# Kernel tuning notes

Hardware: AMD Instinct MI355X
Metric: run time of the kernel (lower is better)

Reference implementation:

```python
import jax, jax.numpy as jnp
import numpy as np
import math

IN_FEATURES = 1024
OUT_FEATURES = 1024
GRID_SIZE = 5
SPLINE_ORDER = 3
BATCH = 4096
K = GRID_SIZE + 2 * SPLINE_ORDER  # 11 basis functions per feature


def make_grid():
    h = (1.0 - (-1.0)) / GRID_SIZE
    xx = np.arange(-SPLINE_ORDER, GRID_SIZE + SPLINE_ORDER + 1, dtype=np.float32) * h + (-1.0)
    return jnp.asarray(np.broadcast_to(xx, (IN_FEATURES, xx.shape[0])).copy())  # (in, K+1)


def setup_inputs() -> dict:
    key = jax.random.key(0)
    k1, k2, k3, k4 = jax.random.split(key, 4)
    x = jax.random.normal(k1, (BATCH, IN_FEATURES), dtype=jnp.float32)
    base_weight = jax.random.normal(k2, (OUT_FEATURES, IN_FEATURES), dtype=jnp.float32) * 0.02
    spline_weight = jax.random.normal(k3, (OUT_FEATURES, IN_FEATURES, K), dtype=jnp.float32) * 0.02
    spline_scaler = jax.random.normal(k4, (OUT_FEATURES, IN_FEATURES), dtype=jnp.float32) * 0.1
    return {"x": x, "base_weight": base_weight, "spline_weight": spline_weight,
            "spline_scaler": spline_scaler, "grid": make_grid()}


def trig_basis(x, grid):
    # x: (B, in) ; grid: (in, K+1) -> basis: (B, in, K)
    a = grid[:, :-1]                      # (in, K)
    b = grid[:, 1:]                       # (in, K)
    interval = jnp.maximum(b - a, 1e-8)
    xe = x[:, :, None]                    # (B, in, 1)
    inside = ((xe >= a) & (xe < b)).astype(x.dtype)
    trig = jnp.sin(jnp.pi * (xe - a) / interval)
    return inside * trig


def reference(x, base_weight, spline_weight, spline_scaler, grid):
    # base branch: SiLU(x) @ base_weight^T
    enm = jax.nn.silu(x) @ base_weight.T                     # (B, out)
    # spline branch: fused basis expansion + GEMM
    basis = trig_basis(x, grid)                              # (B, in, K)
    sw = spline_weight * spline_scaler[:, :, None]           # (out, in, K)
    snm = jnp.einsum('bik,oik->bo', basis, sw)               # (B, out)
    return enm + snm
```

## Files before the change

kernel.cpp:

```cpp
#include <hip/hip_runtime.h>
#include <hip/hip_bf16.h>

#define BATCH  4096
#define INF    1024
#define OUTF   1024
#define KSPL   11
#define KSPB   11264
#define SW_SCALE 1016.0f

using bf16    = __hip_bfloat16;
using short8  = __attribute__((ext_vector_type(8))) short;
using ushort8 = __attribute__((ext_vector_type(8))) unsigned short;
using f32x4   = __attribute__((ext_vector_type(4))) float;
using i32x4   = __attribute__((ext_vector_type(4))) int;
typedef unsigned long long u64;

__device__ __forceinline__ unsigned short f2bf(float f){
  union { float f; unsigned u; } a; a.f = f;
  return (unsigned short)((a.u + 0x7FFFu + ((a.u >> 16) & 1u)) >> 16);
}

__device__ __forceinline__ void llds16(const void* g, const void* l){
  __builtin_amdgcn_global_load_lds(
      (const __attribute__((address_space(1))) unsigned int*)g,
      (__attribute__((address_space(3))) unsigned int*)l, 16, 0, 0);
}

__device__ __forceinline__ void bar(){
  asm volatile("" ::: "memory");
  __builtin_amdgcn_s_barrier();
  asm volatile("" ::: "memory");
}

__device__ __forceinline__ f32x4 mfma16(short8 a, short8 b, f32x4 c){
  return __builtin_amdgcn_mfma_f32_16x16x32_bf16(a, b, c, 0, 0, 0);
}
__device__ __forceinline__ i32x4 mfma_i8(i32x4 a, i32x4 b, i32x4 c){
  return __builtin_amdgcn_mfma_i32_16x16x64_i8(a, b, c, 0, 0, 0);
}

__device__ __forceinline__ int swz(int L){ return L ^ (((L>>7)&7)<<4); }

__global__ __launch_bounds__(256) void prep(const float* __restrict__ x,
                                            const float* __restrict__ bw,
                                            const float* __restrict__ sw,
                                            const float* __restrict__ sc,
                                            bf16* __restrict__ A_sil,
                                            char* __restrict__ A_spl,
                                            bf16* __restrict__ W_b,
                                            char* __restrict__ W_s){
  const int t = threadIdx.x;
  if (blockIdx.x < 2048){
    const int gid = blockIdx.x * 256 + t;
    const int b  = gid >> 7;
    const int i0 = (gid & 127) * 8;
    const float* xr = x + (size_t)b * INF + i0;
    f32x4 p0 = *(const f32x4*)xr;
    f32x4 p1 = *(const f32x4*)(xr + 4);
    float v[8];
    #pragma unroll
    for (int j = 0; j < 4; ++j){ v[j] = p0[j]; v[4+j] = p1[j]; }
    ushort8 sl;
    int c[8], q[8];
    #pragma unroll
    for (int j = 0; j < 8; ++j){
      float xx = v[j];
      sl[j] = f2bf(xx / (1.0f + __expf(-xx)));
      float tt = (xx + 1.0f) * 2.5f;
      float fl = floorf(tt);
      c[j] = (int)fl + 3;
      q[j] = (int)rintf(__sinf(3.14159265358979f * (tt - fl)) * 127.0f);
    }
    *(ushort8*)(A_sil + (size_t)b*INF + i0) = sl;
    char* ar = A_spl + (size_t)b * KSPB + i0;
    #pragma unroll
    for (int k = 0; k < KSPL; ++k){
      u64 up = 0;
      #pragma unroll
      for (int j = 0; j < 8; ++j){
        unsigned char byte = (c[j] == k) ? (unsigned char)q[j] : (unsigned char)0;
        up |= ((u64)byte) << (8*j);
      }
      *(u64*)(ar + k*INF) = up;
    }
  } else {
    const int gid = (blockIdx.x - 2048) * 256 + t;
    const int o  = gid >> 7;
    const int i0 = (gid & 127) * 8;
    float buf[88];
    const float* sp = sw + ((size_t)o*INF + i0) * KSPL;
    #pragma unroll
    for (int qd = 0; qd < 22; ++qd)
      ((f32x4*)buf)[qd] = ((const f32x4*)sp)[qd];
    f32x4 c0 = *(const f32x4*)(sc + (size_t)o*INF + i0);
    f32x4 c1 = *(const f32x4*)(sc + (size_t)o*INF + i0 + 4);
    float scv[8];
    #pragma unroll
    for (int j = 0; j < 4; ++j){ scv[j] = c0[j]; scv[4+j] = c1[j]; }
    {
      const float* br = bw + (size_t)o*INF + i0;
      f32x4 v0 = *(const f32x4*)br;
      f32x4 v1 = *(const f32x4*)(br + 4);
      ushort8 u;
      #pragma unroll
      for (int j = 0; j < 4; ++j){ u[j] = f2bf(v0[j]); u[4+j] = f2bf(v1[j]); }
      *(ushort8*)(W_b + (size_t)o*INF + i0) = u;
    }
    char* wr = W_s + (size_t)o * KSPB + i0;
    #pragma unroll
    for (int k = 0; k < KSPL; ++k){
      u64 up = 0;
      #pragma unroll
      for (int j = 0; j < 8; ++j){
        float vv = buf[j*KSPL + k] * scv[j] * SW_SCALE;
        vv = fminf(fmaxf(vv, -127.0f), 127.0f);
        int qq = (int)rintf(vv);
        up |= ((u64)(unsigned char)(signed char)qq) << (8*j);
      }
      *(u64*)(wr + k*INF) = up;
    }
  }
}

template<int NS>
__global__ __launch_bounds__(512, 2) void gemm_i8k(const char* __restrict__ A,
                                                   const char* __restrict__ W,
                                                   int* __restrict__ Cp){
  constexpr int KSPLIT_B = KSPB / NS;
  constexpr int NG       = KSPLIT_B / 64;
  __shared__ __align__(16) char smem[131072];

  const int bid = blockIdx.x;
  const int xcd = bid & 7, local = bid >> 3;
  const int split = xcd >> 1;
  const int mt    = (xcd & 1) * 8 + (local >> 2);
  const int nt    = local & 3;
  const int bm = mt*256, bn = nt*256;

  const int t    = threadIdx.x;
  const int lane = t & 63, w = t >> 6;
  const int wr = w >> 2, wc = w & 3;
  const int r15 = lane & 15, hi = lane >> 4;

  int offA[8], offB[4];
  #pragma unroll
  for (int m = 0; m < 8; ++m){
    int L = (wr*128 + m*16 + r15)*64 + hi*16;
    offA[m] = swz(L);
  }
  #pragma unroll
  for (int n = 0; n < 4; ++n){
    int L = (wc*64 + n*16 + r15)*64 + hi*16;
    offB[n] = 16384 + swz(L);
  }

  const char* gA[2]; const char* gB[2];
  int ldsA[2], ldsB[2];
  #pragma unroll
  for (int j = 0; j < 2; ++j){
    int P = (t + j*512)*16;
    int L = swz(P);
    int row = L >> 6, inner = L & 63;
    gA[j] = A + (size_t)(bm + row)*KSPB + split*KSPLIT_B + inner;
    gB[j] = W + (size_t)(bn + row)*KSPB + split*KSPLIT_B + inner;
    ldsA[j] = j*8192 + w*1024;
    ldsB[j] = 16384 + j*8192 + w*1024;
  }

  #define STAGE(buf, tile) do{ \
    llds16(gA[0] + (tile)*64, smem + (buf)*32768 + ldsA[0]); \
    llds16(gA[1] + (tile)*64, smem + (buf)*32768 + ldsA[1]); \
    llds16(gB[0] + (tile)*64, smem + (buf)*32768 + ldsB[0]); \
    llds16(gB[1] + (tile)*64, smem + (buf)*32768 + ldsB[1]); }while(0)

  i32x4 acc[8][4] = {};
  i32x4 afA[4], afB[4], bfA[4], bfB[4];

  STAGE(0,0);
  STAGE(1,1);
  asm volatile("s_waitcnt vmcnt(4)" ::: "memory");
  bar();
  #pragma unroll
  for (int n = 0; n < 4; ++n) bfA[n] = *(const i32x4*)(smem + offB[n]);
  #pragma unroll
  for (int m = 0; m < 4; ++m) afA[m] = *(const i32x4*)(smem + offA[m]);

  #define BODY(tt, curA, curB, nxtA, nxtB) do{                                \
    const char* bp_ = smem + ((tt)&3)*32768;                                  \
    const char* bq_ = smem + (((tt)+1)&3)*32768;                              \
    if ((tt) + 2 < NG){                                                       \
      STAGE(((tt)+2)&3, (tt)+2);                                              \
      asm volatile("s_waitcnt vmcnt(4)" ::: "memory");                        \
    } else {                                                                  \
      asm volatile("s_waitcnt vmcnt(0)" ::: "memory");                        \
    }                                                                         \
    bar();                                                                    \
    i32x4 ag_[4];                                                             \
    __builtin_amdgcn_s_setprio(1);                                            \
    _Pragma("unroll")                                                         \
    for (int m = 0; m < 4; ++m){                                              \
      ag_[m] = *(const i32x4*)(bp_ + offA[4+m]);                              \
      _Pragma("unroll")                                                       \
      for (int n = 0; n < 4; ++n)                                             \
        acc[m][n] = mfma_i8(curA[m], curB[n], acc[m][n]);                     \
    }                                                                         \
    _Pragma("unroll")                                                         \
    for (int m = 0; m < 4; ++m){                                              \
      if ((tt) + 1 < NG){                                                     \
        nxtA[m] = *(const i32x4*)(bq_ + offA[m]);                             \
        nxtB[m] = *(const i32x4*)(bq_ + offB[m]);                             \
      }                                                                       \
      _Pragma("unroll")                                                       \
      for (int n = 0; n < 4; ++n)                                             \
        acc[4+m][n] = mfma_i8(ag_[m], curB[n], acc[4+m][n]);                  \
    }                                                                         \
    __builtin_amdgcn_s_setprio(0);                                            \
  }while(0)

  #pragma unroll 1
  for (int s = 0; s < NG/2; ++s){
    BODY(2*s,   afA, bfA, afB, bfB);
    BODY(2*s+1, afB, bfB, afA, bfA);
  }
  #undef BODY
  #undef STAGE

  int* outp = Cp + (size_t)split * (BATCH*OUTF);
  #pragma unroll
  for (int m = 0; m < 8; ++m){
    const int r0 = bm + wr*128 + m*16 + hi*4;
    #pragma unroll
    for (int n = 0; n < 4; ++n){
      const int cc = bn + wc*64 + n*16 + r15;
      #pragma unroll
      for (int j = 0; j < 4; ++j)
        outp[(size_t)(r0 + j) * OUTF + cc] = acc[m][n][j];
    }
  }
}

__global__ __launch_bounds__(512, 2) void gemm_e(const bf16* __restrict__ A,
                                                 const bf16* __restrict__ W,
                                                 const int* __restrict__ Cp,
                                                 float* __restrict__ out){
  constexpr int NG = 32;
  __shared__ __align__(16) char smem[65536];

  const int bid = blockIdx.x;
  const int fin = (bid & 7) * 32 + (bid >> 3);
  const int mt = fin >> 3, nt = fin & 7;
  const int bm = mt*128, bn = nt*128;

  const int t    = threadIdx.x;
  const int lane = t & 63, w = t >> 6;
  const int wr = w >> 2, wc = w & 3;
  const int r15 = lane & 15, hi = lane >> 4;

  int offA[4], offB[2];
  #pragma unroll
  for (int m = 0; m < 4; ++m){
    int L = (wr*64 + m*16 + r15)*64 + hi*16;
    offA[m] = swz(L);
  }
  #pragma unroll
  for (int n = 0; n < 2; ++n){
    int L = (wc*32 + n*16 + r15)*64 + hi*16;
    offB[n] = 8192 + swz(L);
  }

  const char* gA; const char* gB;
  {
    int P = t*16;
    int L = swz(P);
    int row = L >> 6, inner = L & 63;
    gA = (const char*)A + (size_t)(bm + row)*2048 + inner;
    gB = (const char*)W + (size_t)(bn + row)*2048 + inner;
  }
  const int ldsA = w*1024;
  const int ldsB = 8192 + w*1024;

  #define STAGE(buf, tile) do{ \
    llds16(gA + (tile)*64, smem + (buf)*16384 + ldsA); \
    llds16(gB + (tile)*64, smem + (buf)*16384 + ldsB); }while(0)

  f32x4 acc[4][2] = {};
  short8 afA[4], afB[4], bfA[2], bfB[2];

  STAGE(0,0);
  STAGE(1,1);
  asm volatile("s_waitcnt vmcnt(2)" ::: "memory");
  bar();
  #pragma unroll
  for (int m = 0; m < 4; ++m) afA[m] = *(const short8*)(smem + offA[m]);
  #pragma unroll
  for (int n = 0; n < 2; ++n) bfA[n] = *(const short8*)(smem + offB[n]);

  #define BODY(tt, curA, curB, nxtA, nxtB) do{                                \
    const char* bq_ = smem + (((tt)+1)&3)*16384;                              \
    if ((tt) + 2 < NG){                                                       \
      STAGE(((tt)+2)&3, (tt)+2);                                              \
      asm volatile("s_waitcnt vmcnt(2)" ::: "memory");                        \
    } else {                                                                  \
      asm volatile("s_waitcnt vmcnt(0)" ::: "memory");                        \
    }                                                                         \
    bar();                                                                    \
    __builtin_amdgcn_s_setprio(1);                                            \
    _Pragma("unroll")                                                         \
    for (int m = 0; m < 4; ++m){                                              \
      if ((tt) + 1 < NG){                                                     \
        nxtA[m] = *(const short8*)(bq_ + offA[m]);                            \
        if (m < 2) nxtB[m] = *(const short8*)(bq_ + offB[m]);                 \
      }                                                                       \
      _Pragma("unroll")                                                       \
      for (int n = 0; n < 2; ++n)                                             \
        acc[m][n] = mfma16(curA[m], curB[n], acc[m][n]);                      \
    }                                                                         \
    __builtin_amdgcn_s_setprio(0);                                            \
  }while(0)

  #pragma unroll 1
  for (int s = 0; s < NG/2; ++s){
    BODY(2*s,   afA, bfA, afB, bfB);
    BODY(2*s+1, afB, bfB, afA, bfA);
  }
  #undef BODY
  #undef STAGE

  const float invP = 1.0f / (127.0f * SW_SCALE);
  const size_t NN = (size_t)BATCH * OUTF;
  #pragma unroll
  for (int m = 0; m < 4; ++m){
    const int r0 = bm + wr*64 + m*16 + hi*4;
    #pragma unroll
    for (int n = 0; n < 2; ++n){
      const int cc = bn + wc*32 + n*16 + r15;
      #pragma unroll
      for (int j = 0; j < 4; ++j){
        const size_t idx = (size_t)(r0 + j) * OUTF + cc;
        int s4 = Cp[idx] + Cp[NN + idx] + Cp[2*NN + idx] + Cp[3*NN + idx];
        out[idx] = acc[m][n][j] + (float)s4 * invP;
      }
    }
  }
}

__global__ __launch_bounds__(256) void fallback(const float* __restrict__ x,
    const float* __restrict__ bw, const float* __restrict__ sw,
    const float* __restrict__ sc, float* __restrict__ out){
  const int b = blockIdx.x, t = threadIdx.x;
  __shared__ float ls[INF], sg[INF];
  __shared__ int   lc[INF];
  for (int i = t; i < INF; i += 256){
    float xx = x[(size_t)b*INF + i];
    ls[i] = xx / (1.0f + __expf(-xx));
    float tt = (xx + 1.0f)*2.5f;
    float fl = floorf(tt);
    int c = (int)fl + 3;
    lc[i] = ((unsigned)c < 11u) ? c : -1;
    sg[i] = __sinf(3.14159265358979f*(tt - fl));
  }
  __syncthreads();
  for (int o = t; o < OUTF; o += 256){
    float acc = 0.f;
    const float* bwr = bw + (size_t)o*INF;
    const float* swr = sw + (size_t)o*INF*KSPL;
    const float* scr = sc + (size_t)o*INF;
    for (int i = 0; i < INF; ++i){
      acc = fmaf(ls[i], bwr[i], acc);
      int c = lc[i];
      if (c >= 0) acc = fmaf(sg[i]*scr[i], swr[i*KSPL + c], acc);
    }
    out[(size_t)b*OUTF + o] = acc;
  }
}

extern "C" void kernel_launch(void* const* d_in, const int* in_sizes, int n_in,
                              void* d_out, int out_size, void* d_ws, size_t ws_size,
                              hipStream_t stream){
  const float* x  = (const float*)d_in[0];
  const float* bw = (const float*)d_in[1];
  const float* sw = (const float*)d_in[2];
  const float* sc = (const float*)d_in[3];
  float* out = (float*)d_out;
  const size_t oAsil = 0;
  const size_t oAspl = oAsil + (size_t)BATCH*INF*2;
  const size_t oWb   = oAspl + (size_t)BATCH*KSPB;
  const size_t oWs   = oWb   + (size_t)OUTF*INF*2;
  const size_t oCp   = oWs   + (size_t)OUTF*KSPB;
  const size_t total = oCp   + (size_t)4*BATCH*OUTF*4;
  if (ws_size >= total){
    bf16* A_sil = (bf16*)((char*)d_ws + oAsil);
    char* A_spl = (char*)d_ws + oAspl;
    bf16* W_b   = (bf16*)((char*)d_ws + oWb);
    char* W_s   = (char*)d_ws + oWs;
    int*  Cp    = (int*)((char*)d_ws + oCp);
    hipLaunchKernelGGL(prep, dim3(2560), dim3(256), 0, stream,
                       x, bw, sw, sc, A_sil, A_spl, W_b, W_s);
    gemm_i8k<4><<<dim3(256), dim3(512), 0, stream>>>(A_spl, W_s, Cp);
    gemm_e<<<dim3(256), dim3(512), 0, stream>>>(A_sil, W_b, Cp, out);
  } else {
    hipLaunchKernelGGL(fallback, dim3(BATCH), dim3(256), 0, stream, x, bw, sw, sc, out);
  }
}
```

Baseline: 101.7 us.

## Halve int8 spline GEMM tile to 128x256 with triple-buffered LDS and more blocks

Shrinks the int8 split-K GEMM block tile from 256x256 to 128x256 and doubles the grid to 512 blocks. LDS use drops from 128KB to 72KB with a 3-buffer ring, and launch bounds rise to allow 4 blocks per CU. The register double-buffered fragment prefetch is replaced by a simpler loop that loads fragments after the barrier and adds a second barrier per iteration. The aim is more occupancy and better CU fill, at the cost of less reuse per block, more global traffic for W, and extra synchronisation.

```diff
diff --git a/kernel.cpp b/kernel.cpp
--- a/kernel.cpp
+++ b/kernel.cpp
@@ -123,112 +123,99 @@
 }
 
 template<int NS>
-__global__ __launch_bounds__(512, 2) void gemm_i8k(const char* __restrict__ A,
+__global__ __launch_bounds__(512, 4) void gemm_i8b(const char* __restrict__ A,
                                                    const char* __restrict__ W,
                                                    int* __restrict__ Cp){
   constexpr int KSPLIT_B = KSPB / NS;
   constexpr int NG       = KSPLIT_B / 64;
-  __shared__ __align__(16) char smem[131072];
+  constexpr int BUFSZ    = 24576;
+  __shared__ __align__(16) char smem[3*BUFSZ];
 
   const int bid = blockIdx.x;
   const int xcd = bid & 7, local = bid >> 3;
   const int split = xcd >> 1;
-  const int mt    = (xcd & 1) * 8 + (local >> 2);
+  const int mt    = (xcd & 1) * 16 + (local >> 2);
   const int nt    = local & 3;
-  const int bm = mt*256, bn = nt*256;
+  const int bm = mt*128, bn = nt*256;
 
   const int t    = threadIdx.x;
   const int lane = t & 63, w = t >> 6;
   const int wr = w >> 2, wc = w & 3;
   const int r15 = lane & 15, hi = lane >> 4;
 
-  int offA[8], offB[4];
-  #pragma unroll
-  for (int m = 0; m < 8; ++m){
-    int L = (wr*128 + m*16 + r15)*64 + hi*16;
+  int offA[4], offB[4];
+  #pragma unroll
+  for (int m = 0; m < 4; ++m){
+    int L = (wr*64 + m*16 + r15)*64 + hi*16;
     offA[m] = swz(L);
   }
   #pragma unroll
   for (int n = 0; n < 4; ++n){
     int L = (wc*64 + n*16 + r15)*64 + hi*16;
-    offB[n] = 16384 + swz(L);
-  }
-
-  const char* gA[2]; const char* gB[2];
-  int ldsA[2], ldsB[2];
+    offB[n] = 8192 + swz(L);
+  }
+
+  const char* gA; const char* gB[2];
+  int ldsA, ldsB[2];
+  {
+    int P = t*16;
+    int L = swz(P);
+    gA   = A + (size_t)(bm + (L>>6))*KSPB + split*KSPLIT_B + (L & 63);
+    ldsA = w*1024;
+  }
   #pragma unroll
   for (int j = 0; j < 2; ++j){
-    int P = (t + j*512)*16;
+    int P = t*16 + j*8192;
     int L = swz(P);
-    int row = L >> 6, inner = L & 63;
-    gA[j] = A + (size_t)(bm + row)*KSPB + split*KSPLIT_B + inner;
-    gB[j] = W + (size_t)(bn + row)*KSPB + split*KSPLIT_B + inner;
-    ldsA[j] = j*8192 + w*1024;
-    ldsB[j] = 16384 + j*8192 + w*1024;
+    gB[j]   = W + (size_t)(bn + (L>>6))*KSPB + split*KSPLIT_B + (L & 63);
+    ldsB[j] = 8192 + j*8192 + w*1024;
   }
 
   #define STAGE(buf, tile) do{ \
-    llds16(gA[0] + (tile)*64, smem + (buf)*32768 + ldsA[0]); \
-    llds16(gA[1] + (tile)*64, smem + (buf)*32768 + ldsA[1]); \
-    llds16(gB[0] + (tile)*64, smem + (buf)*32768 + ldsB[0]); \
-    llds16(gB[1] + (tile)*64, smem + (buf)*32768 + ldsB[1]); }while(0)
-
-  i32x4 acc[8][4] = {};
-  i32x4 afA[4], afB[4], bfA[4], bfB[4];
+    llds16(gA    + (tile)*64, smem + (buf)*BUFSZ + ldsA); \
+    llds16(gB[0] + (tile)*64, smem + (buf)*BUFSZ + ldsB[0]); \
+    llds16(gB[1] + (tile)*64, smem + (buf)*BUFSZ + ldsB[1]); }while(0)
+
+  i32x4 acc[4][4] = {};
 
   STAGE(0,0);
   STAGE(1,1);
-  asm volatile("s_waitcnt vmcnt(4)" ::: "memory");
+  asm volatile("s_waitcnt vmcnt(3)" ::: "memory");
   bar();
-  #pragma unroll
-  for (int n = 0; n < 4; ++n) bfA[n] = *(const i32x4*)(smem + offB[n]);
-  #pragma unroll
-  for (int m = 0; m < 4; ++m) afA[m] = *(const i32x4*)(smem + offA[m]);
-
-  #define BODY(tt, curA, curB, nxtA, nxtB) do{                                \
-    const char* bp_ = smem + ((tt)&3)*32768;                                  \
-    const char* bq_ = smem + (((tt)+1)&3)*32768;                              \
-    if ((tt) + 2 < NG){                                                       \
-      STAGE(((tt)+2)&3, (tt)+2);                                              \
-      asm volatile("s_waitcnt vmcnt(4)" ::: "memory");                        \
-    } else {                                                                  \
-      asm volatile("s_waitcnt vmcnt(0)" ::: "memory");                        \
-    }                                                                         \
-    bar();                                                                    \
-    i32x4 ag_[4];                                                             \
-    __builtin_amdgcn_s_setprio(1);                                            \
-    _Pragma("unroll")                                                         \
-    for (int m = 0; m < 4; ++m){                                              \
-      ag_[m] = *(const i32x4*)(bp_ + offA[4+m]);                              \
-      _Pragma("unroll")                                                       \
-      for (int n = 0; n < 4; ++n)                                             \
-        acc[m][n] = mfma_i8(curA[m], curB[n], acc[m][n]);                     \
-    }                                                                         \
-    _Pragma("unroll")                                                         \
-    for (int m = 0; m < 4; ++m){                                              \
-      if ((tt) + 1 < NG){                                                     \
-        nxtA[m] = *(const i32x4*)(bq_ + offA[m]);                             \
-        nxtB[m] = *(const i32x4*)(bq_ + offB[m]);                             \
-      }                                                                       \
-      _Pragma("unroll")                                                       \
-      for (int n = 0; n < 4; ++n)                                             \
-        acc[4+m][n] = mfma_i8(ag_[m], curB[n], acc[4+m][n]);                  \
-    }                                                                         \
-    __builtin_amdgcn_s_setprio(0);                                            \
-  }while(0)
-
+
+  int cur = 0;
   #pragma unroll 1
-  for (int s = 0; s < NG/2; ++s){
-    BODY(2*s,   afA, bfA, afB, bfB);
-    BODY(2*s+1, afB, bfB, afA, bfA);
-  }
-  #undef BODY
+  for (int tt = 0; tt < NG; ++tt){
+    if (tt + 2 < NG){
+      int sb = cur + 2; if (sb >= 3) sb -= 3;
+      STAGE(sb, tt+2);
+      asm volatile("s_waitcnt vmcnt(3)" ::: "memory");
+    } else {
+      asm volatile("s_waitcnt vmcnt(0)" ::: "memory");
+    }
+    bar();
+    const char* bp = smem + cur*BUFSZ;
+    i32x4 af[4], bf[4];
+    #pragma unroll
+    for (int m = 0; m < 4; ++m) af[m] = *(const i32x4*)(bp + offA[m]);
+    #pragma unroll
+    for (int n = 0; n < 4; ++n) bf[n] = *(const i32x4*)(bp + offB[n]);
+    __builtin_amdgcn_s_setprio(1);
+    #pragma unroll
+    for (int m = 0; m < 4; ++m)
+      #pragma unroll
+      for (int n = 0; n < 4; ++n)
+        acc[m][n] = mfma_i8(af[m], bf[n], acc[m][n]);
+    __builtin_amdgcn_s_setprio(0);
+    bar();
+    ++cur; if (cur == 3) cur = 0;
+  }
   #undef STAGE
 
   int* outp = Cp + (size_t)split * (BATCH*OUTF);
   #pragma unroll
-  for (int m = 0; m < 8; ++m){
-    const int r0 = bm + wr*128 + m*16 + hi*4;
+  for (int m = 0; m < 4; ++m){
+    const int r0 = bm + wr*64 + m*16 + hi*4;
     #pragma unroll
     for (int n = 0; n < 4; ++n){
       const int cc = bn + wc*64 + n*16 + r15;
@@ -396,7 +383,7 @@
     int*  Cp    = (int*)((char*)d_ws + oCp);
     hipLaunchKernelGGL(prep, dim3(2560), dim3(256), 0, stream,
                        x, bw, sw, sc, A_sil, A_spl, W_b, W_s);
-    gemm_i8k<4><<<dim3(256), dim3(512), 0, stream>>>(A_spl, W_s, Cp);
+    gemm_i8b<4><<<dim3(512), dim3(512), 0, stream>>>(A_spl, W_s, Cp);
     gemm_e<<<dim3(256), dim3(512), 0, stream>>>(A_sil, W_b, Cp, out);
   } else {
     hipLaunchKernelGGL(fallback, dim3(BATCH), dim3(256), 0, stream, x, bw, sw, sc, out);
```

New measurement: 111.4 us. 1.1x slower.
